# Optimization experiments

Hardware: AMD Instinct MI355X
Metric: run time of the kernel (lower is better)

The kernel has to match this reference:

```python
import jax, jax.numpy as jnp
import numpy as np

NUM_HEADS = 4
HEAD_DIM = 32
QUERY_DIM = 256
KEY_DIM = 128
INNER = NUM_HEADS * HEAD_DIM  # 128


def setup_inputs() -> dict:
    key = jax.random.key(0)
    ks = jax.random.split(key, 8)
    B, T, D, H, W = 2, 4, QUERY_DIM, 40, 40
    C, Hm, Wm = KEY_DIM, 40, 40
    query = jax.random.normal(ks[0], (B, T, D, H, W), dtype=jnp.float32)
    k_in = jax.random.normal(ks[1], (B, T, C, Hm, Wm), dtype=jnp.float32)
    v_in = jax.random.normal(ks[2], (B, T, C, Hm, Wm), dtype=jnp.float32)
    # Linear weights stored as (in, out); torch nn.Linear init ~ U(-1/sqrt(in), 1/sqrt(in))
    def lin(k, fan_in, fan_out):
        bound = 1.0 / np.sqrt(fan_in)
        return jax.random.uniform(k, (fan_in, fan_out), minval=-bound, maxval=bound, dtype=jnp.float32)
    Wq = lin(ks[3], QUERY_DIM, INNER)
    Wk = lin(ks[4], KEY_DIM, INNER)
    Wv = lin(ks[5], KEY_DIM, INNER)
    Wo = lin(ks[6], INNER, QUERY_DIM)
    bo = jax.random.uniform(ks[7], (QUERY_DIM,), minval=-1.0 / np.sqrt(INNER), maxval=1.0 / np.sqrt(INNER), dtype=jnp.float32)
    return {"query": query, "key": k_in, "value": v_in,
            "Wq": Wq, "Wk": Wk, "Wv": Wv, "Wo": Wo, "bo": bo}


def reference(query, key, value, Wq, Wk, Wv, Wo, bo):
    B, T, D, H, W = query.shape
    _, _, C, Hm, Wm = key.shape
    scale = HEAD_DIM ** (-0.5)
    # b t d h w -> b t (h w) d
    q = query.reshape(B, T, D, H * W).transpose(0, 1, 3, 2)
    k = key.reshape(B, T, C, Hm * Wm).transpose(0, 1, 3, 2)
    v = value.reshape(B, T, C, Hm * Wm).transpose(0, 1, 3, 2)
    # projections then split heads: b t n (h d) -> b t h n d
    def heads(x):
        Bn, Tn, N, _ = x.shape
        return x.reshape(Bn, Tn, N, NUM_HEADS, HEAD_DIM).transpose(0, 1, 3, 2, 4)
    Q = heads(q @ Wq)
    K = heads(k @ Wk)
    V = heads(v @ Wv)
    scores = jnp.einsum('bthqd,bthkd->bthqk', Q, K) * scale
    probs = jax.nn.softmax(scores, axis=-1)
    out = jnp.einsum('bthqk,bthkd->bthqd', probs, V)
    # b t h n d -> b t n (h d)
    out = out.transpose(0, 1, 3, 2, 4).reshape(B, T, H * W, INNER)
    fused = out @ Wo + bo
    # b t (h w) d -> b t d h w
    return fused.transpose(0, 1, 3, 2).reshape(B, T, D, H, W)
```

## Files before the change

kernel.cpp:

```cpp
#include <hip/hip_runtime.h>

#define NTOK 1600
#define BT_TOTAL 8
#define INNER 128
#define HD 32
#define NH 4
#define QDIM 256

typedef short short8 __attribute__((ext_vector_type(8)));
typedef short short4v __attribute__((ext_vector_type(4)));
typedef float f32x2 __attribute__((ext_vector_type(2)));
typedef float f32x4 __attribute__((ext_vector_type(4)));
typedef float f32x16 __attribute__((ext_vector_type(16)));
typedef unsigned uint2v __attribute__((ext_vector_type(2)));

__device__ inline short f2b(float x) {
  union { float f; unsigned u; } v; v.f = x;
  unsigned r = (v.u + 0x7FFF + ((v.u >> 16) & 1)) >> 16;
  return (short)r;
}
__device__ inline unsigned cvtpk(float a, float b) {
  unsigned r;
  asm("v_cvt_pk_bf16_f32 %0, %1, %2" : "=v"(r) : "v"(a), "v"(b));
  return r;
}
__device__ inline void pswap(unsigned &a, unsigned &b) {
  uint2v r = __builtin_amdgcn_permlane32_swap(a, b, false, false);
  a = r[0]; b = r[1];
}
__device__ inline short8 ldsfrag(const short* p) {
  short4v a = *(const short4v*)p;
  short4v b = *(const short4v*)(p + 4);
  short8 r;
  r[0] = a[0]; r[1] = a[1]; r[2] = a[2]; r[3] = a[3];
  r[4] = b[0]; r[5] = b[1]; r[6] = b[2]; r[7] = b[3];
  return r;
}
__device__ inline short8 mk8(unsigned a, unsigned b, unsigned c, unsigned d) {
  union { unsigned u[4]; short8 v; } t;
  t.u[0] = a; t.u[1] = b; t.u[2] = c; t.u[3] = d;
  return t.v;
}

__global__ __launch_bounds__(256) void proj_fused(
    const float* __restrict__ query, const float* __restrict__ Wq,
    const float* __restrict__ key, const float* __restrict__ Wk,
    const float* __restrict__ value, const float* __restrict__ Wv,
    short* __restrict__ Qbf, short* __restrict__ Kbf,
    short* __restrict__ Vbf) {
  const int n0 = blockIdx.x * 64;
  const int which = blockIdx.y;
  const int bt = blockIdx.z;
  const int t = threadIdx.x;
  const int lane = t & 63, w = t >> 6;
  const int quad = lane >> 4, n16 = lane & 15;

  const float* X; const float* Wt; short* Y; int nchunk; float scl;
  if (which == 0) {
    X = query; Wt = Wq; Y = Qbf; nchunk = 8;
    scl = 0.17677669529663687f * 1.4426950408889634f;
  } else if (which == 1) {
    X = key; Wt = Wk; Y = Kbf; nchunk = 4; scl = 1.0f;
  } else {
    X = value; Wt = Wv; Y = Vbf; nchunk = 4; scl = 1.0f;
  }
  const float* Xb = X + (size_t)bt * (nchunk * 32) * NTOK;

  __shared__ short Xs[64 * 36];
  __shared__ short Ws[128 * 36];

  f32x4 acc[8];
#pragma unroll
  for (int i = 0; i < 8; ++i) acc[i] = (f32x4){0.f, 0.f, 0.f, 0.f};

  const int iw = t & 127, g = t >> 7;

  float xf0[4], xf1[4], wf0[8], wf1[8];
  auto loadX = [&](int cd) {
#pragma unroll
    for (int dp = 0; dp < 4; ++dp) {
      int dl = w * 8 + dp * 2;
      xf0[dp] = Xb[(size_t)(cd + dl) * NTOK + n0 + lane];
      xf1[dp] = Xb[(size_t)(cd + dl + 1) * NTOK + n0 + lane];
    }
  };
  auto loadW = [&](int cd) {
#pragma unroll
    for (int dp = 0; dp < 8; ++dp) {
      int dl = g * 16 + dp * 2;
      wf0[dp] = Wt[(size_t)(cd + dl) * INNER + iw];
      wf1[dp] = Wt[(size_t)(cd + dl + 1) * INNER + iw];
    }
  };
  loadX(0); loadW(0);

  for (int c = 0; c < nchunk; ++c) {
#pragma unroll
    for (int dp = 0; dp < 4; ++dp)
      *(unsigned*)&Xs[lane * 36 + w * 8 + dp * 2] = cvtpk(xf0[dp], xf1[dp]);
#pragma unroll
    for (int dp = 0; dp < 8; ++dp)
      *(unsigned*)&Ws[iw * 36 + g * 16 + dp * 2] = cvtpk(wf0[dp], wf1[dp]);
    __syncthreads();
    if (c + 1 < nchunk) { loadX((c + 1) * 32); loadW((c + 1) * 32); }
    if (which != 2) {
      short8 a[4], b[2];
#pragma unroll
      for (int tg = 0; tg < 4; ++tg)
        a[tg] = ldsfrag(&Xs[(tg * 16 + n16) * 36 + quad * 8]);
#pragma unroll
      for (int cg = 0; cg < 2; ++cg)
        b[cg] = ldsfrag(&Ws[(w * 32 + cg * 16 + n16) * 36 + quad * 8]);
#pragma unroll
      for (int tg = 0; tg < 4; ++tg)
#pragma unroll
        for (int cg = 0; cg < 2; ++cg)
          acc[tg * 2 + cg] = __builtin_amdgcn_mfma_f32_16x16x32_bf16(
              a[tg], b[cg], acc[tg * 2 + cg], 0, 0, 0);
    } else {
      short8 a[2], b[4];
#pragma unroll
      for (int ig = 0; ig < 2; ++ig)
        a[ig] = ldsfrag(&Ws[(w * 32 + ig * 16 + n16) * 36 + quad * 8]);
#pragma unroll
      for (int tg = 0; tg < 4; ++tg)
        b[tg] = ldsfrag(&Xs[(tg * 16 + n16) * 36 + quad * 8]);
#pragma unroll
      for (int ig = 0; ig < 2; ++ig)
#pragma unroll
        for (int tg = 0; tg < 4; ++tg)
          acc[ig * 4 + tg] = __builtin_amdgcn_mfma_f32_16x16x32_bf16(
              a[ig], b[tg], acc[ig * 4 + tg], 0, 0, 0);
    }
    __syncthreads();
  }

  if (which != 2) {
    short* Yb = Y + ((size_t)bt * NH + w) * NTOK * HD;
#pragma unroll
    for (int tg = 0; tg < 4; ++tg)
#pragma unroll
      for (int cg = 0; cg < 2; ++cg) {
        f32x4 a = acc[tg * 2 + cg];
#pragma unroll
        for (int r = 0; r < 4; ++r) {
          int tok = n0 + tg * 16 + quad * 4 + r;
          Yb[(size_t)tok * HD + cg * 16 + n16] = f2b(a[r] * scl);
        }
      }
  } else {
#pragma unroll
    for (int ig = 0; ig < 2; ++ig)
#pragma unroll
      for (int tg = 0; tg < 4; ++tg) {
        f32x4 a = acc[ig * 4 + tg];
#pragma unroll
        for (int r = 0; r < 4; ++r) {
          int irow = w * 32 + ig * 16 + quad * 4 + r;
          Y[((size_t)bt * INNER + irow) * NTOK + n0 + tg * 16 + n16] =
              f2b(a[r]);
        }
      }
  }
}

__global__ __launch_bounds__(256, 5) void attn_mfma(
    const short* __restrict__ Qb, const short* __restrict__ Kb,
    const short* __restrict__ Vb, short* __restrict__ Obf) {
  const int id = blockIdx.x;
  const int qt = id >> 5;
  const int pair = id & 31;
  const int bt = pair >> 2, h = pair & 3;
  const int wave = threadIdx.x >> 6, lane = threadIdx.x & 63;
  const int lh = lane >> 5, q32 = lane & 31;
  const int q0 = qt * 32;
  const size_t btok = ((size_t)bt * NH + h) * NTOK;
  const size_t bd = ((size_t)bt * NH + h) * HD;

  __shared__ float Cb[2][17][64];

  const short* Qp = &Qb[(btok + q0 + q32) * HD + lh * 8];
  const short8 bq0 = *(const short8*)(Qp);
  const short8 bq1 = *(const short8*)(Qp + 16);

  const int kstart = wave * 416 - (wave == 3 ? 32 : 0);
  const int nch = 13 - (wave >> 1);
  const short* Kp = &Kb[(btok + kstart + q32) * HD + lh * 8];
  const short* Vp = &Vb[(bd + q32) * NTOK + kstart + lh * 8];

  f32x16 o = {0.f, 0.f, 0.f, 0.f, 0.f, 0.f, 0.f, 0.f,
              0.f, 0.f, 0.f, 0.f, 0.f, 0.f, 0.f, 0.f};
  f32x2 ls2 = {0.f, 0.f};

  short8 ak0 = *(const short8*)(Kp);
  short8 ak1 = *(const short8*)(Kp + 16);
  short8 av0 = *(const short8*)(Vp);
  short8 av1 = *(const short8*)(Vp + 16);

  for (int i = 0; i < nch; ++i) {
    const int kn = (i + 1 < nch) ? (i + 1) * 32 : 0;
    short8 nk0 = *(const short8*)(Kp + (size_t)kn * HD);
    short8 nk1 = *(const short8*)(Kp + (size_t)kn * HD + 16);
    short8 nv0 = *(const short8*)(Vp + kn);
    short8 nv1 = *(const short8*)(Vp + kn + 16);

    __builtin_amdgcn_s_setprio(1);
    f32x16 s = __builtin_amdgcn_mfma_f32_32x32x16_bf16(
        ak0, bq0,
        (f32x16){0.f, 0.f, 0.f, 0.f, 0.f, 0.f, 0.f, 0.f,
                 0.f, 0.f, 0.f, 0.f, 0.f, 0.f, 0.f, 0.f},
        0, 0, 0);
    s = __builtin_amdgcn_mfma_f32_32x32x16_bf16(ak1, bq1, s, 0, 0, 0);
    __builtin_amdgcn_s_setprio(0);

    unsigned Pd[8];
#pragma unroll
    for (int g = 0; g < 4; ++g) {
      float e0 = __builtin_amdgcn_exp2f(s[4 * g + 0]);
      float e1 = __builtin_amdgcn_exp2f(s[4 * g + 1]);
      float e2 = __builtin_amdgcn_exp2f(s[4 * g + 2]);
      float e3 = __builtin_amdgcn_exp2f(s[4 * g + 3]);
      ls2 += (f32x2){e0, e1};
      ls2 += (f32x2){e2, e3};
      Pd[2 * g + 0] = cvtpk(e0, e1);
      Pd[2 * g + 1] = cvtpk(e2, e3);
    }
    pswap(Pd[0], Pd[2]);
    pswap(Pd[1], Pd[3]);
    pswap(Pd[4], Pd[6]);
    pswap(Pd[5], Pd[7]);
    short8 pb0 = mk8(Pd[0], Pd[1], Pd[2], Pd[3]);
    short8 pb1 = mk8(Pd[4], Pd[5], Pd[6], Pd[7]);

    __builtin_amdgcn_s_setprio(1);
    o = __builtin_amdgcn_mfma_f32_32x32x16_bf16(av0, pb0, o, 0, 0, 0);
    o = __builtin_amdgcn_mfma_f32_32x32x16_bf16(av1, pb1, o, 0, 0, 0);
    __builtin_amdgcn_s_setprio(0);

    ak0 = nk0; ak1 = nk1; av0 = nv0; av1 = nv1;
  }

  float lsum = ls2[0] + ls2[1];
  lsum += __shfl_xor(lsum, 32);

  auto dump = [&](int sidx) {
#pragma unroll
    for (int r = 0; r < 16; ++r) Cb[sidx][r][lane] = o[r];
    Cb[sidx][16][lane] = lsum;
  };
  auto accum = [&](int sidx) {
#pragma unroll
    for (int r = 0; r < 16; ++r) o[r] += Cb[sidx][r][lane];
    lsum += Cb[sidx][16][lane];
  };
  if (wave == 1) dump(0);
  if (wave == 3) dump(1);
  __syncthreads();
  if (wave == 0) accum(0);
  if (wave == 2) accum(1);
  __syncthreads();
  if (wave == 2) dump(0);
  __syncthreads();
  if (wave == 0) {
    accum(0);
    const float inv = 1.f / lsum;
    short* Op = &Obf[((size_t)bt * NTOK + q0 + q32) * INNER + h * HD + lh * 4];
#pragma unroll
    for (int g = 0; g < 4; ++g) {
      unsigned d0 = cvtpk(o[4 * g + 0] * inv, o[4 * g + 1] * inv);
      unsigned d1 = cvtpk(o[4 * g + 2] * inv, o[4 * g + 3] * inv);
      *(uint2*)&Op[8 * g] = make_uint2(d0, d1);
    }
  }
}

__global__ __launch_bounds__(256) void oproj_mfma(
    const short* __restrict__ Obf, const float* __restrict__ Wo,
    const float* __restrict__ bo, float* __restrict__ out) {
  const int tok0 = blockIdx.x * 64, d0 = blockIdx.y * 64;
  const int bt = blockIdx.z;
  const int t = threadIdx.x, lane = t & 63, w = t >> 6;
  const int quad = lane >> 4, n16 = lane & 15;
  __shared__ short Wos[64 * 36];
  f32x4 acc[4];
#pragma unroll
  for (int i = 0; i < 4; ++i) acc[i] = (f32x4){0.f, 0.f, 0.f, 0.f};
  const int tok = tok0 + w * 16 + n16;

  float wf0[4], wf1[4];
  short8 bfr;
  auto loadWo = [&](int c) {
#pragma unroll
    for (int dp = 0; dp < 4; ++dp) {
      int il = w * 8 + dp * 2;
      wf0[dp] = Wo[(size_t)(c * 32 + il) * QDIM + d0 + lane];
      wf1[dp] = Wo[(size_t)(c * 32 + il + 1) * QDIM + d0 + lane];
    }
  };
  auto loadB = [&](int c) {
    bfr = *(const short8*)&Obf[((size_t)bt * NTOK + tok) * INNER + c * 32 +
                               quad * 8];
  };
  loadWo(0); loadB(0);

  for (int c = 0; c < 4; ++c) {
#pragma unroll
    for (int dp = 0; dp < 4; ++dp)
      *(unsigned*)&Wos[lane * 36 + w * 8 + dp * 2] = cvtpk(wf0[dp], wf1[dp]);
    __syncthreads();
    short8 b0 = bfr;
    if (c < 3) { loadWo(c + 1); loadB(c + 1); }
#pragma unroll
    for (int ag = 0; ag < 4; ++ag) {
      short8 a = ldsfrag(&Wos[(ag * 16 + n16) * 36 + quad * 8]);
      acc[ag] = __builtin_amdgcn_mfma_f32_16x16x32_bf16(a, b0, acc[ag], 0, 0, 0);
    }
    __syncthreads();
  }

#pragma unroll
  for (int ag = 0; ag < 4; ++ag) {
    f32x4 a = acc[ag];
#pragma unroll
    for (int r = 0; r < 4; ++r) {
      int dout = d0 + ag * 16 + quad * 4 + r;
      out[((size_t)bt * QDIM + dout) * NTOK + tok] = a[r] + bo[dout];
    }
  }
}

extern "C" void kernel_launch(void* const* d_in, const int* in_sizes, int n_in,
                              void* d_out, int out_size, void* d_ws,
                              size_t ws_size, hipStream_t stream) {
  const float* query = (const float*)d_in[0];
  const float* key = (const float*)d_in[1];
  const float* value = (const float*)d_in[2];
  const float* Wq = (const float*)d_in[3];
  const float* Wk = (const float*)d_in[4];
  const float* Wv = (const float*)d_in[5];
  const float* Wo = (const float*)d_in[6];
  const float* bo = (const float*)d_in[7];
  float* out = (float*)d_out;

  const size_t arr = (size_t)BT_TOTAL * INNER * NTOK;
  short* Qbf = (short*)d_ws;
  short* Kbf = Qbf + arr;
  short* Vbf = Kbf + arr;
  short* Obf = Vbf + arr;

  proj_fused<<<dim3(25, 3, BT_TOTAL), 256, 0, stream>>>(
      query, Wq, key, Wk, value, Wv, Qbf, Kbf, Vbf);
  attn_mfma<<<dim3(1600), 256, 0, stream>>>(Qbf, Kbf, Vbf, Obf);
  oproj_mfma<<<dim3(25, 4, BT_TOTAL), 256, 0, stream>>>(Obf, Wo, bo, out);
}
```

Baseline: 133.3 us.

## Software-pipeline attention loop so QK MFMA overlaps softmax of previous chunk

```diff
diff --git a/kernel.cpp b/kernel.cpp
--- a/kernel.cpp
+++ b/kernel.cpp
@@ -164,7 +164,7 @@
   }
 }
 
-__global__ __launch_bounds__(256, 5) void attn_mfma(
+__global__ __launch_bounds__(256, 4) void attn_mfma(
     const short* __restrict__ Qb, const short* __restrict__ Kb,
     const short* __restrict__ Vb, short* __restrict__ Obf) {
   const int id = blockIdx.x;
@@ -192,34 +192,14 @@
               0.f, 0.f, 0.f, 0.f, 0.f, 0.f, 0.f, 0.f};
   f32x2 ls2 = {0.f, 0.f};
 
-  short8 ak0 = *(const short8*)(Kp);
-  short8 ak1 = *(const short8*)(Kp + 16);
-  short8 av0 = *(const short8*)(Vp);
-  short8 av1 = *(const short8*)(Vp + 16);
-
-  for (int i = 0; i < nch; ++i) {
-    const int kn = (i + 1 < nch) ? (i + 1) * 32 : 0;
-    short8 nk0 = *(const short8*)(Kp + (size_t)kn * HD);
-    short8 nk1 = *(const short8*)(Kp + (size_t)kn * HD + 16);
-    short8 nv0 = *(const short8*)(Vp + kn);
-    short8 nv1 = *(const short8*)(Vp + kn + 16);
-
-    __builtin_amdgcn_s_setprio(1);
-    f32x16 s = __builtin_amdgcn_mfma_f32_32x32x16_bf16(
-        ak0, bq0,
-        (f32x16){0.f, 0.f, 0.f, 0.f, 0.f, 0.f, 0.f, 0.f,
-                 0.f, 0.f, 0.f, 0.f, 0.f, 0.f, 0.f, 0.f},
-        0, 0, 0);
-    s = __builtin_amdgcn_mfma_f32_32x32x16_bf16(ak1, bq1, s, 0, 0, 0);
-    __builtin_amdgcn_s_setprio(0);
-
+  auto softmax_pack = [&](const f32x16& sv, short8& pb0, short8& pb1) {
     unsigned Pd[8];
 #pragma unroll
     for (int g = 0; g < 4; ++g) {
-      float e0 = __builtin_amdgcn_exp2f(s[4 * g + 0]);
-      float e1 = __builtin_amdgcn_exp2f(s[4 * g + 1]);
-      float e2 = __builtin_amdgcn_exp2f(s[4 * g + 2]);
-      float e3 = __builtin_amdgcn_exp2f(s[4 * g + 3]);
+      float e0 = __builtin_amdgcn_exp2f(sv[4 * g + 0]);
+      float e1 = __builtin_amdgcn_exp2f(sv[4 * g + 1]);
+      float e2 = __builtin_amdgcn_exp2f(sv[4 * g + 2]);
+      float e3 = __builtin_amdgcn_exp2f(sv[4 * g + 3]);
       ls2 += (f32x2){e0, e1};
       ls2 += (f32x2){e2, e3};
       Pd[2 * g + 0] = cvtpk(e0, e1);
@@ -229,15 +209,61 @@
     pswap(Pd[1], Pd[3]);
     pswap(Pd[4], Pd[6]);
     pswap(Pd[5], Pd[7]);
-    short8 pb0 = mk8(Pd[0], Pd[1], Pd[2], Pd[3]);
-    short8 pb1 = mk8(Pd[4], Pd[5], Pd[6], Pd[7]);
-
-    __builtin_amdgcn_s_setprio(1);
-    o = __builtin_amdgcn_mfma_f32_32x32x16_bf16(av0, pb0, o, 0, 0, 0);
-    o = __builtin_amdgcn_mfma_f32_32x32x16_bf16(av1, pb1, o, 0, 0, 0);
-    __builtin_amdgcn_s_setprio(0);
-
-    ak0 = nk0; ak1 = nk1; av0 = nv0; av1 = nv1;
+    pb0 = mk8(Pd[0], Pd[1], Pd[2], Pd[3]);
+    pb1 = mk8(Pd[4], Pd[5], Pd[6], Pd[7]);
+  };
+
+  const f32x16 zero16 = {0.f, 0.f, 0.f, 0.f, 0.f, 0.f, 0.f, 0.f,
+                         0.f, 0.f, 0.f, 0.f, 0.f, 0.f, 0.f, 0.f};
+  auto kidx = [&](int c) -> size_t { return (c < nch) ? (size_t)c * 32 : 0; };
+
+  short8 kA0 = *(const short8*)(Kp);
+  short8 kA1 = *(const short8*)(Kp + 16);
+  short8 vA0 = *(const short8*)(Vp);
+  short8 vA1 = *(const short8*)(Vp + 16);
+  short8 kB0 = *(const short8*)(Kp + (size_t)32 * HD);
+  short8 kB1 = *(const short8*)(Kp + (size_t)32 * HD + 16);
+  short8 vB0 = *(const short8*)(Vp + 32);
+  short8 vB1 = *(const short8*)(Vp + 32 + 16);
+
+  f32x16 s = __builtin_amdgcn_mfma_f32_32x32x16_bf16(kA0, bq0, zero16, 0, 0, 0);
+  s = __builtin_amdgcn_mfma_f32_32x32x16_bf16(kA1, bq1, s, 0, 0, 0);
+  f32x16 s2;
+  short8 pb0, pb1;
+
+  const int npair = nch >> 1;
+#pragma unroll 1
+  for (int tp = 0; tp < npair; ++tp) {
+    const int c = 2 * tp;
+    {
+      const size_t kn = kidx(c + 2);
+      kA0 = *(const short8*)(Kp + kn * HD);
+      kA1 = *(const short8*)(Kp + kn * HD + 16);
+      softmax_pack(s, pb0, pb1);
+      s2 = __builtin_amdgcn_mfma_f32_32x32x16_bf16(kB0, bq0, zero16, 0, 0, 0);
+      s2 = __builtin_amdgcn_mfma_f32_32x32x16_bf16(kB1, bq1, s2, 0, 0, 0);
+      o = __builtin_amdgcn_mfma_f32_32x32x16_bf16(vA0, pb0, o, 0, 0, 0);
+      o = __builtin_amdgcn_mfma_f32_32x32x16_bf16(vA1, pb1, o, 0, 0, 0);
+      vA0 = *(const short8*)(Vp + kn);
+      vA1 = *(const short8*)(Vp + kn + 16);
+    }
+    {
+      const size_t kn = kidx(c + 3);
+      kB0 = *(const short8*)(Kp + kn * HD);
+      kB1 = *(const short8*)(Kp + kn * HD + 16);
+      softmax_pack(s2, pb0, pb1);
+      s = __builtin_amdgcn_mfma_f32_32x32x16_bf16(kA0, bq0, zero16, 0, 0, 0);
+      s = __builtin_amdgcn_mfma_f32_32x32x16_bf16(kA1, bq1, s, 0, 0, 0);
+      o = __builtin_amdgcn_mfma_f32_32x32x16_bf16(vB0, pb0, o, 0, 0, 0);
+      o = __builtin_amdgcn_mfma_f32_32x32x16_bf16(vB1, pb1, o, 0, 0, 0);
+      vB0 = *(const short8*)(Vp + kn);
+      vB1 = *(const short8*)(Vp + kn + 16);
+    }
+  }
+  if (nch & 1) {
+    softmax_pack(s, pb0, pb1);
+    o = __builtin_amdgcn_mfma_f32_32x32x16_bf16(vA0, pb0, o, 0, 0, 0);
+    o = __builtin_amdgcn_mfma_f32_32x32x16_bf16(vA1, pb1, o, 0, 0, 0);
   }
 
   float lsum = ls2[0] + ls2[1];
```

After: 134.8 us. Within noise of the previous version (+1.1%).

## Process two 32-query tiles per attention block to reuse K/V fragments

Applied to the files above, without the earlier changes.

```diff
diff --git a/kernel.cpp b/kernel.cpp
--- a/kernel.cpp
+++ b/kernel.cpp
@@ -164,7 +164,7 @@
   }
 }
 
-__global__ __launch_bounds__(256, 5) void attn_mfma(
+__global__ __launch_bounds__(256, 3) void attn_mfma(
     const short* __restrict__ Qb, const short* __restrict__ Kb,
     const short* __restrict__ Vb, short* __restrict__ Obf) {
   const int id = blockIdx.x;
@@ -173,24 +173,50 @@
   const int bt = pair >> 2, h = pair & 3;
   const int wave = threadIdx.x >> 6, lane = threadIdx.x & 63;
   const int lh = lane >> 5, q32 = lane & 31;
-  const int q0 = qt * 32;
+  const int q0 = qt * 64;
   const size_t btok = ((size_t)bt * NH + h) * NTOK;
   const size_t bd = ((size_t)bt * NH + h) * HD;
 
-  __shared__ float Cb[2][17][64];
-
-  const short* Qp = &Qb[(btok + q0 + q32) * HD + lh * 8];
-  const short8 bq0 = *(const short8*)(Qp);
-  const short8 bq1 = *(const short8*)(Qp + 16);
+  __shared__ float Cb[2][2][17][64];
+
+  const short* QpA = &Qb[(btok + q0 + q32) * HD + lh * 8];
+  const short* QpB = QpA + 32 * HD;
+  const short8 bqA0 = *(const short8*)(QpA);
+  const short8 bqA1 = *(const short8*)(QpA + 16);
+  const short8 bqB0 = *(const short8*)(QpB);
+  const short8 bqB1 = *(const short8*)(QpB + 16);
 
   const int kstart = wave * 416 - (wave == 3 ? 32 : 0);
   const int nch = 13 - (wave >> 1);
   const short* Kp = &Kb[(btok + kstart + q32) * HD + lh * 8];
   const short* Vp = &Vb[(bd + q32) * NTOK + kstart + lh * 8];
 
-  f32x16 o = {0.f, 0.f, 0.f, 0.f, 0.f, 0.f, 0.f, 0.f,
-              0.f, 0.f, 0.f, 0.f, 0.f, 0.f, 0.f, 0.f};
-  f32x2 ls2 = {0.f, 0.f};
+  const f32x16 zero16 = {0.f, 0.f, 0.f, 0.f, 0.f, 0.f, 0.f, 0.f,
+                         0.f, 0.f, 0.f, 0.f, 0.f, 0.f, 0.f, 0.f};
+  f32x16 oA = zero16, oB = zero16;
+  f32x2 lsA = {0.f, 0.f}, lsB = {0.f, 0.f};
+
+  auto softmax_pack = [&](const f32x16& sv, f32x2& ls2, short8& pb0,
+                          short8& pb1) {
+    unsigned Pd[8];
+#pragma unroll
+    for (int g = 0; g < 4; ++g) {
+      float e0 = __builtin_amdgcn_exp2f(sv[4 * g + 0]);
+      float e1 = __builtin_amdgcn_exp2f(sv[4 * g + 1]);
+      float e2 = __builtin_amdgcn_exp2f(sv[4 * g + 2]);
+      float e3 = __builtin_amdgcn_exp2f(sv[4 * g + 3]);
+      ls2 += (f32x2){e0, e1};
+      ls2 += (f32x2){e2, e3};
+      Pd[2 * g + 0] = cvtpk(e0, e1);
+      Pd[2 * g + 1] = cvtpk(e2, e3);
+    }
+    pswap(Pd[0], Pd[2]);
+    pswap(Pd[1], Pd[3]);
+    pswap(Pd[4], Pd[6]);
+    pswap(Pd[5], Pd[7]);
+    pb0 = mk8(Pd[0], Pd[1], Pd[2], Pd[3]);
+    pb1 = mk8(Pd[4], Pd[5], Pd[6], Pd[7]);
+  };
 
   short8 ak0 = *(const short8*)(Kp);
   short8 ak1 = *(const short8*)(Kp + 16);
@@ -198,78 +224,74 @@
   short8 av1 = *(const short8*)(Vp + 16);
 
   for (int i = 0; i < nch; ++i) {
-    const int kn = (i + 1 < nch) ? (i + 1) * 32 : 0;
-    short8 nk0 = *(const short8*)(Kp + (size_t)kn * HD);
-    short8 nk1 = *(const short8*)(Kp + (size_t)kn * HD + 16);
+    const size_t kn = (i + 1 < nch) ? (size_t)(i + 1) * 32 : 0;
+    short8 nk0 = *(const short8*)(Kp + kn * HD);
+    short8 nk1 = *(const short8*)(Kp + kn * HD + 16);
     short8 nv0 = *(const short8*)(Vp + kn);
     short8 nv1 = *(const short8*)(Vp + kn + 16);
 
-    __builtin_amdgcn_s_setprio(1);
-    f32x16 s = __builtin_amdgcn_mfma_f32_32x32x16_bf16(
-        ak0, bq0,
-        (f32x16){0.f, 0.f, 0.f, 0.f, 0.f, 0.f, 0.f, 0.f,
-                 0.f, 0.f, 0.f, 0.f, 0.f, 0.f, 0.f, 0.f},
-        0, 0, 0);
-    s = __builtin_amdgcn_mfma_f32_32x32x16_bf16(ak1, bq1, s, 0, 0, 0);
-    __builtin_amdgcn_s_setprio(0);
-
-    unsigned Pd[8];
-#pragma unroll
-    for (int g = 0; g < 4; ++g) {
-      float e0 = __builtin_amdgcn_exp2f(s[4 * g + 0]);
-      float e1 = __builtin_amdgcn_exp2f(s[4 * g + 1]);
-      float e2 = __builtin_amdgcn_exp2f(s[4 * g + 2]);
-      float e3 = __builtin_amdgcn_exp2f(s[4 * g + 3]);
-      ls2 += (f32x2){e0, e1};
-      ls2 += (f32x2){e2, e3};
-      Pd[2 * g + 0] = cvtpk(e0, e1);
-      Pd[2 * g + 1] = cvtpk(e2, e3);
-    }
-    pswap(Pd[0], Pd[2]);
-    pswap(Pd[1], Pd[3]);
-    pswap(Pd[4], Pd[6]);
-    pswap(Pd[5], Pd[7]);
-    short8 pb0 = mk8(Pd[0], Pd[1], Pd[2], Pd[3]);
-    short8 pb1 = mk8(Pd[4], Pd[5], Pd[6], Pd[7]);
-
-    __builtin_amdgcn_s_setprio(1);
-    o = __builtin_amdgcn_mfma_f32_32x32x16_bf16(av0, pb0, o, 0, 0, 0);
-    o = __builtin_amdgcn_mfma_f32_32x32x16_bf16(av1, pb1, o, 0, 0, 0);
-    __builtin_amdgcn_s_setprio(0);
+    f32x16 sA = __builtin_amdgcn_mfma_f32_32x32x16_bf16(ak0, bqA0, zero16,
+                                                        0, 0, 0);
+    sA = __builtin_amdgcn_mfma_f32_32x32x16_bf16(ak1, bqA1, sA, 0, 0, 0);
+    f32x16 sB = __builtin_amdgcn_mfma_f32_32x32x16_bf16(ak0, bqB0, zero16,
+                                                        0, 0, 0);
+    sB = __builtin_amdgcn_mfma_f32_32x32x16_bf16(ak1, bqB1, sB, 0, 0, 0);
+
+    short8 pbA0, pbA1, pbB0, pbB1;
+    softmax_pack(sA, lsA, pbA0, pbA1);
+    softmax_pack(sB, lsB, pbB0, pbB1);
+
+    oA = __builtin_amdgcn_mfma_f32_32x32x16_bf16(av0, pbA0, oA, 0, 0, 0);
+    oA = __builtin_amdgcn_mfma_f32_32x32x16_bf16(av1, pbA1, oA, 0, 0, 0);
+    oB = __builtin_amdgcn_mfma_f32_32x32x16_bf16(av0, pbB0, oB, 0, 0, 0);
+    oB = __builtin_amdgcn_mfma_f32_32x32x16_bf16(av1, pbB1, oB, 0, 0, 0);
 
     ak0 = nk0; ak1 = nk1; av0 = nv0; av1 = nv1;
   }
 
-  float lsum = ls2[0] + ls2[1];
-  lsum += __shfl_xor(lsum, 32);
-
-  auto dump = [&](int sidx) {
-#pragma unroll
-    for (int r = 0; r < 16; ++r) Cb[sidx][r][lane] = o[r];
-    Cb[sidx][16][lane] = lsum;
-  };
-  auto accum = [&](int sidx) {
-#pragma unroll
-    for (int r = 0; r < 16; ++r) o[r] += Cb[sidx][r][lane];
-    lsum += Cb[sidx][16][lane];
-  };
-  if (wave == 1) dump(0);
-  if (wave == 3) dump(1);
+  float lsumA = lsA[0] + lsA[1];
+  lsumA += __shfl_xor(lsumA, 32);
+  float lsumB = lsB[0] + lsB[1];
+  lsumB += __shfl_xor(lsumB, 32);
+
+  auto dump = [&](int tl, int sidx, const f32x16& o, float ls) {
+#pragma unroll
+    for (int r = 0; r < 16; ++r) Cb[tl][sidx][r][lane] = o[r];
+    Cb[tl][sidx][16][lane] = ls;
+  };
+  auto accum = [&](int tl, int sidx, f32x16& o, float& ls) {
+#pragma unroll
+    for (int r = 0; r < 16; ++r) o[r] += Cb[tl][sidx][r][lane];
+    ls += Cb[tl][sidx][16][lane];
+  };
+  if (wave == 1) { dump(0, 0, oA, lsumA); dump(1, 0, oB, lsumB); }
+  if (wave == 3) { dump(0, 1, oA, lsumA); dump(1, 1, oB, lsumB); }
   __syncthreads();
-  if (wave == 0) accum(0);
-  if (wave == 2) accum(1);
+  if (wave == 0) { accum(0, 0, oA, lsumA); accum(1, 0, oB, lsumB); }
+  if (wave == 2) { accum(0, 1, oA, lsumA); accum(1, 1, oB, lsumB); }
   __syncthreads();
-  if (wave == 2) dump(0);
+  if (wave == 2) { dump(0, 0, oA, lsumA); dump(1, 0, oB, lsumB); }
   __syncthreads();
   if (wave == 0) {
-    accum(0);
-    const float inv = 1.f / lsum;
-    short* Op = &Obf[((size_t)bt * NTOK + q0 + q32) * INNER + h * HD + lh * 4];
+    accum(0, 0, oA, lsumA);
+    accum(1, 0, oB, lsumB);
+    const float invA = 1.f / lsumA;
+    short* OpA =
+        &Obf[((size_t)bt * NTOK + q0 + q32) * INNER + h * HD + lh * 4];
 #pragma unroll
     for (int g = 0; g < 4; ++g) {
-      unsigned d0 = cvtpk(o[4 * g + 0] * inv, o[4 * g + 1] * inv);
-      unsigned d1 = cvtpk(o[4 * g + 2] * inv, o[4 * g + 3] * inv);
-      *(uint2*)&Op[8 * g] = make_uint2(d0, d1);
+      unsigned d0 = cvtpk(oA[4 * g + 0] * invA, oA[4 * g + 1] * invA);
+      unsigned d1 = cvtpk(oA[4 * g + 2] * invA, oA[4 * g + 3] * invA);
+      *(uint2*)&OpA[8 * g] = make_uint2(d0, d1);
+    }
+    const float invB = 1.f / lsumB;
+    short* OpB =
+        &Obf[((size_t)bt * NTOK + q0 + 32 + q32) * INNER + h * HD + lh * 4];
+#pragma unroll
+    for (int g = 0; g < 4; ++g) {
+      unsigned d0 = cvtpk(oB[4 * g + 0] * invB, oB[4 * g + 1] * invB);
+      unsigned d1 = cvtpk(oB[4 * g + 2] * invB, oB[4 * g + 3] * invB);
+      *(uint2*)&OpB[8 * g] = make_uint2(d0, d1);
     }
   }
 }
@@ -350,6 +372,6 @@
 
   proj_fused<<<dim3(25, 3, BT_TOTAL), 256, 0, stream>>>(
       query, Wq, key, Wk, value, Wv, Qbf, Kbf, Vbf);
-  attn_mfma<<<dim3(1600), 256, 0, stream>>>(Qbf, Kbf, Vbf, Obf);
+  attn_mfma<<<dim3(800), 256, 0, stream>>>(Qbf, Kbf, Vbf, Obf);
   oproj_mfma<<<dim3(25, 4, BT_TOTAL), 256, 0, stream>>>(Obf, Wo, bo, out);
 }
```

New measurement: 120.3 us (median of 2 runs). 9.8% less time.
